# Optimization experiments

Hardware: AMD Instinct MI355X
Metric: run time of the kernel (lower is better)

## Reference

```python
import jax, jax.numpy as jnp
import numpy as np
from jax import lax

B, T, D, H, Z, L = 64, 1024, 128, 512, 64, 2

def lstm_layer(x_tbd, h0, c0, Wih, Whh, bih, bhh):
    # x_tbd: [T,B,Din]; precompute input contribution (big GEMM outside scan)
    gx = jnp.einsum('tbd,gd->tbg', x_tbd, Wih) + (bih + bhh)  # [T,B,4H]
    def step(carry, gxt):
        h, c = carry
        gates = gxt + h @ Whh.T
        i, f, g, o = jnp.split(gates, 4, axis=-1)
        c = jax.nn.sigmoid(f) * c + jax.nn.sigmoid(i) * jnp.tanh(g)
        h = jax.nn.sigmoid(o) * jnp.tanh(c)
        return (h, c), h
    (hT, cT), hs = lax.scan(step, (h0, c0), gx)
    return hs, hT, cT  # hs: [T,B,H]

def run_lstm(x_btd, h0_l, c0_l, params):
    # params: list of (Wih, Whh, bih, bhh) per layer; h0_l/c0_l: [L,B,H]
    seq = jnp.transpose(x_btd, (1, 0, 2))
    hTs = []
    for l, (Wih, Whh, bih, bhh) in enumerate(params):
        seq, hT, cT = lstm_layer(seq, h0_l[l], c0_l[l], Wih, Whh, bih, bhh)
        hTs.append(hT)
    return jnp.transpose(seq, (1, 0, 2)), jnp.stack(hTs)

def setup_inputs() -> dict:
    key = jax.random.key(0)
    ks = iter(jax.random.split(key, 32))
    s = 0.05
    d = {'x': jax.random.uniform(next(ks), (B, T, D), jnp.float32)}
    for pre in ('enc', 'dec'):
        for l in range(L):
            din = D if l == 0 else H
            d[f'{pre}_Wih{l}'] = jax.random.normal(next(ks), (4 * H, din), jnp.float32) * s
            d[f'{pre}_Whh{l}'] = jax.random.normal(next(ks), (4 * H, H), jnp.float32) * s
            d[f'{pre}_bih{l}'] = jnp.zeros((4 * H,), jnp.float32)
            d[f'{pre}_bhh{l}'] = jnp.zeros((4 * H,), jnp.float32)
    d['tl_W'] = jax.random.normal(next(ks), (Z, H), jnp.float32) * s
    d['tl_b'] = jnp.zeros((Z,), jnp.float32)
    d['lh_W'] = jax.random.normal(next(ks), (H * L, Z), jnp.float32) * s
    d['lh_b'] = jnp.zeros((H * L,), jnp.float32)
    d['op_W'] = jax.random.normal(next(ks), (D, H), jnp.float32) * s
    d['op_b'] = jnp.zeros((D,), jnp.float32)
    return d

def reference(x, enc_Wih0, enc_Whh0, enc_bih0, enc_bhh0, enc_Wih1, enc_Whh1, enc_bih1, enc_bhh1,
              dec_Wih0, dec_Whh0, dec_bih0, dec_bhh0, dec_Wih1, dec_Whh1, dec_bih1, dec_bhh1,
              tl_W, tl_b, lh_W, lh_b, op_W, op_b):
    enc_p = [(enc_Wih0, enc_Whh0, enc_bih0, enc_bhh0), (enc_Wih1, enc_Whh1, enc_bih1, enc_bhh1)]
    dec_p = [(dec_Wih0, dec_Whh0, dec_bih0, dec_bhh0), (dec_Wih1, dec_Whh1, dec_bih1, dec_bhh1)]
    zeros_lbh = jnp.zeros((L, B, H), x.dtype)
    # encode
    _, h_n = run_lstm(x, zeros_lbh, zeros_lbh, enc_p)
    z = h_n[-1] @ tl_W.T + tl_b  # [B,Z]
    # decode: zero input sequence, latent-derived initial hidden state
    init_h = jnp.tanh(z @ lh_W.T + lh_b).reshape(B, L, H).transpose(1, 0, 2)  # matches torch .view(L,B,H)? no
    init_h = jnp.tanh(z @ lh_W.T + lh_b).reshape(L, B, H)  # torch: view(num_layers, batch, hidden) on [B, H*L] flat -- faithful to source
    dec_in = jnp.zeros((B, T, D), x.dtype)
    dec_out, _ = run_lstm(dec_in, init_h, jnp.zeros_like(init_h), dec_p)
    recon = jax.nn.sigmoid(jnp.einsum('bth,dh->btd', dec_out, op_W) + op_b)
    return recon, z
```

## Files before the change

kernel.cpp:

```cpp
#include <hip/hip_runtime.h>
#include <cstdint>
#include <cstddef>

typedef unsigned short u16;
typedef unsigned int u32;
typedef __attribute__((ext_vector_type(8))) short short8;
typedef __attribute__((ext_vector_type(4))) float f32x4;

#define AGENT_SCOPE __HIP_MEMORY_SCOPE_AGENT
#define SPIN_CAP 20000000
#define POLL_CAP 200000
#define SENT 0xFFFFFFFFu

__device__ __forceinline__ u16 f2bf(float f) {
  u32 u = __float_as_uint(f);
  return (u16)((u + 0x7FFFu + ((u >> 16) & 1u)) >> 16);
}
__device__ __forceinline__ float bf2f(u16 s) { return __uint_as_float(((u32)s) << 16); }
__device__ __forceinline__ float sigm(float x) { return 1.f / (1.f + __expf(-x)); }
__device__ __forceinline__ float tanha(float x) { return 1.f - 2.f / (__expf(2.f * x) + 1.f); }
__device__ __forceinline__ void wait_vm0() { asm volatile("s_waitcnt vmcnt(0)" ::: "memory"); }
__device__ __forceinline__ u32 um(u32 a, u32 b) { return a > b ? a : b; }

__device__ __forceinline__ uint4 ldx4(const void* p) {
  uint4 r;
  asm volatile("global_load_dwordx4 %0, %1, off sc0 sc1" : "=v"(r) : "v"(p) : "memory");
  return r;
}

__global__ void __launch_bounds__(256, 1)
lstm_ae_kernel(const float* __restrict__ x,
    const float* __restrict__ eWih0, const float* __restrict__ eWhh0,
    const float* __restrict__ ebi0,  const float* __restrict__ ebh0,
    const float* __restrict__ eWih1, const float* __restrict__ eWhh1,
    const float* __restrict__ ebi1,  const float* __restrict__ ebh1,
    const float* __restrict__ dWhh0,
    const float* __restrict__ dbi0,  const float* __restrict__ dbh0,
    const float* __restrict__ dWih1, const float* __restrict__ dWhh1,
    const float* __restrict__ dbi1,  const float* __restrict__ dbh1,
    const float* __restrict__ tlW,   const float* __restrict__ tlb,
    const float* __restrict__ lhW,   const float* __restrict__ lhb,
    const float* __restrict__ opW,   const float* __restrict__ opb,
    float* __restrict__ out, char* __restrict__ wsb)
{
  __shared__ __align__(16) u16 sH0[16 * 520];
  __shared__ __align__(16) u16 sH1[16 * 520];
  __shared__ __align__(16) u16 sX[16 * 136];
  __shared__ __align__(16) u16 sOPW[2 * 520];
  __shared__ float sP[4 * 256];
  __shared__ float sBias[64];
  __shared__ float sC[256];
  __shared__ float sZ[16 * 64];
  __shared__ float sOPB[4];

  u32* gcnt  = (u32*)wsb;
  float* zbuf= (float*)(wsb + 4096);
  u32* h0r   = (u32*)(wsb + 32768);
  u32* h1r   = (u32*)(wsb + 229376);

  const int tid  = threadIdx.x;
  const int col  = blockIdx.x & 3;
  const int rowg = blockIdx.x >> 2;
  const int wid  = tid >> 6;
  const int lane = tid & 63;
  const int m    = lane & 15;
  const int qo   = (lane >> 4) * 8;

  auto stage_slot = [&](int q0, int q1, bool p0on, bool p1on) {
    const char* base0 = (const char*)(h0r + ((q0 * 4 + col) << 12)) + tid * 16;
    const char* base1 = (const char*)(h1r + ((q1 * 4 + col) << 12)) + tid * 16;
    uint4 v0[4], v1[4];
    bool d0 = !p0on, d1 = !p1on;
    int it = 0;
    for (;;) {
      if (!d0) {
        #pragma unroll
        for (int i = 0; i < 4; ++i) v0[i] = ldx4(base0 + i * 4096);
      }
      if (!d1) {
        #pragma unroll
        for (int i = 0; i < 4; ++i) v1[i] = ldx4(base1 + i * 4096);
      }
      asm volatile("s_waitcnt vmcnt(0)" ::: "memory");
      __builtin_amdgcn_sched_barrier(0);
      if (!d0) {
        u32 mx = 0;
        #pragma unroll
        for (int i = 0; i < 4; ++i)
          mx = um(mx, um(um(v0[i].x, v0[i].y), um(v0[i].z, v0[i].w)));
        d0 = (mx != SENT);
      }
      if (!d1) {
        u32 mx = 0;
        #pragma unroll
        for (int i = 0; i < 4; ++i)
          mx = um(mx, um(um(v1[i].x, v1[i].y), um(v1[i].z, v1[i].w)));
        d1 = (mx != SENT);
      }
      if ((d0 && d1) || ++it >= POLL_CAP) break;
      __builtin_amdgcn_s_sleep(4);
    }
    u32* dH0 = (u32*)sH0; u32* dH1 = (u32*)sH1;
    const int db = (tid & 15) * 260 + (tid >> 4) * 4;
    if (p0on) {
      #pragma unroll
      for (int i = 0; i < 4; ++i) *(uint4*)(dH0 + db + i * 64) = v0[i];
    }
    if (p1on) {
      #pragma unroll
      for (int i = 0; i < 4; ++i) *(uint4*)(dH1 + db + i * 64) = v1[i];
    }
  };

  auto clears = [&](int s) {
    if (tid < 64) {
      int cq0 = (s + 1) % 3, cq1 = s % 3;
      __hip_atomic_store(h0r + ((cq0 * 4 + col) << 12) + (rowg << 6) + tid,
                         SENT, __ATOMIC_RELAXED, AGENT_SCOPE);
      __hip_atomic_store(h1r + ((cq1 * 4 + col) << 12) + (rowg << 6) + tid,
                         SENT, __ATOMIC_RELAXED, AGENT_SCOPE);
    }
  };

  auto stage_xt = [&](int s) {
    int b = tid >> 4, seg = tid & 15;
    const float* p = x + (size_t)(col * 16 + b) * 131072 + (size_t)s * 128 + seg * 8;
    float4 f0 = *(const float4*)p, f1 = *(const float4*)(p + 4);
    uint4 v;
    v.x = (u32)f2bf(f0.x) | ((u32)f2bf(f0.y) << 16);
    v.y = (u32)f2bf(f0.z) | ((u32)f2bf(f0.w) << 16);
    v.z = (u32)f2bf(f1.x) | ((u32)f2bf(f1.y) << 16);
    v.w = (u32)f2bf(f1.z) | ((u32)f2bf(f1.w) << 16);
    *(uint4*)(sX + b * 136 + seg * 8) = v;
  };

  auto ldw = [&](const float* W, int ld, int row, int kofs) -> short8 {
    const float* p = W + (size_t)row * ld + kofs + qo;
    float4 f0 = *(const float4*)p, f1 = *(const float4*)(p + 4);
    short8 r;
    r[0] = (short)f2bf(f0.x); r[1] = (short)f2bf(f0.y);
    r[2] = (short)f2bf(f0.z); r[3] = (short)f2bf(f0.w);
    r[4] = (short)f2bf(f1.x); r[5] = (short)f2bf(f1.y);
    r[6] = (short)f2bf(f1.z); r[7] = (short)f2bf(f1.w);
    return r;
  };

  auto act_store = [&](bool L0a, bool L1a, int q0, int q1) {
    int li = tid >> 7, b = (tid >> 3) & 15, u = tid & 7;
    bool actv = li ? L1a : L0a;
    float hv = 0.f;
    if (actv) {
      float gi = sP[(li*2)*256   + b*16 + u]     + sBias[li*32 + u];
      float gf = sP[(li*2)*256   + b*16 + 8 + u] + sBias[li*32 + 8 + u];
      float gg = sP[(li*2+1)*256 + b*16 + u]     + sBias[li*32 + 16 + u];
      float go = sP[(li*2+1)*256 + b*16 + 8 + u] + sBias[li*32 + 24 + u];
      float c = sC[(li*16 + b)*8 + u];
      c = sigm(gf)*c + sigm(gi)*tanha(gg);
      sC[(li*16 + b)*8 + u] = c;
      hv = sigm(go)*tanha(c);
    }
    u16 hb = f2bf(hv);
    u32 other = __shfl_xor((u32)hb, 1);
    if (actv && !(u & 1)) {
      u32 v = (u32)hb | (other << 16);
      u32* ring = li ? h1r : h0r;
      int q = li ? q1 : q0;
      __hip_atomic_store(ring + ((q * 4 + col) << 12) + (rowg << 6) + b * 4 + (u >> 1),
                         v, __ATOMIC_RELAXED, AGENT_SCOPE);
    }
  };

  auto gbar = [&](u32 target) {
    __syncthreads();
    if (tid == 0) {
      __hip_atomic_fetch_add(gcnt, 1u, __ATOMIC_RELEASE, AGENT_SCOPE);
      int it = 0;
      while (__hip_atomic_load(gcnt, __ATOMIC_RELAXED, AGENT_SCOPE) < target && ++it < SPIN_CAP) {}
      (void)__hip_atomic_load(gcnt, __ATOMIC_ACQUIRE, AGENT_SCOPE);
    }
    __syncthreads();
  };

  const int nl = (wid & 1) * 16 + m;
  const int gw = ((nl >> 3) << 9) + rowg * 8 + (nl & 7);

  short8 wb[32];

  if (wid < 2) {
    #pragma unroll
    for (int t = 0; t < 4; ++t)  wb[t]      = ldw(eWih0, 128, gw, t * 32);
    #pragma unroll
    for (int t = 0; t < 16; ++t) wb[4 + t]  = ldw(eWhh0, 512, gw, t * 32);
  } else {
    #pragma unroll
    for (int t = 0; t < 16; ++t) wb[t]      = ldw(eWih1, 512, gw, t * 32);
    #pragma unroll
    for (int t = 0; t < 16; ++t) wb[16 + t] = ldw(eWhh1, 512, gw, t * 32);
  }
  if (tid < 64) {
    int li = tid >> 5, n = tid & 31;
    int g = ((n >> 3) << 9) + rowg * 8 + (n & 7);
    sBias[li * 32 + n] = li ? (ebi1[g] + ebh1[g]) : (ebi0[g] + ebh0[g]);
  }
  sC[tid] = 0.f;
  __syncthreads();

  for (int s = 0; s <= 1024; ++s) {
    const bool L0 = (s < 1024), L1 = (s >= 1);
    if (L0) stage_xt(s);
    stage_slot((s + 2) % 3, (s + 1) % 3, true, s >= 1);
    __syncthreads();
    clears(s);

    f32x4 acc = {0.f, 0.f, 0.f, 0.f};
    if (wid < 2) {
      if (L0) {
        #pragma unroll
        for (int t = 0; t < 4; ++t) {
          short8 a = *(const short8*)(sX + m * 136 + t * 32 + qo);
          acc = __builtin_amdgcn_mfma_f32_16x16x32_bf16(a, wb[t], acc, 0, 0, 0);
        }
        #pragma unroll
        for (int t = 0; t < 16; ++t) {
          short8 a = *(const short8*)(sH0 + m * 520 + t * 32 + qo);
          acc = __builtin_amdgcn_mfma_f32_16x16x32_bf16(a, wb[4 + t], acc, 0, 0, 0);
        }
      }
    } else {
      if (L1) {
        #pragma unroll
        for (int t = 0; t < 16; ++t) {
          short8 a = *(const short8*)(sH0 + m * 520 + t * 32 + qo);
          acc = __builtin_amdgcn_mfma_f32_16x16x32_bf16(a, wb[t], acc, 0, 0, 0);
        }
        #pragma unroll
        for (int t = 0; t < 16; ++t) {
          short8 a = *(const short8*)(sH1 + m * 520 + t * 32 + qo);
          acc = __builtin_amdgcn_mfma_f32_16x16x32_bf16(a, wb[16 + t], acc, 0, 0, 0);
        }
      }
    }
    {
      bool wact = (wid < 2) ? L0 : L1;
      if (wact) {
        int mb = (lane >> 4) * 4;
        #pragma unroll
        for (int r = 0; r < 4; ++r) sP[wid * 256 + (mb + r) * 16 + m] = acc[r];
      }
    }
    __syncthreads();
    {
      wait_vm0();
    }
    act_store(L0, L1, s % 3, (s + 2) % 3);
  }

  {
    const u32* b1 = h1r + ((0 * 4 + col) << 12) + tid;
    u32 v1[16];
    int it = 0; bool ok = false;
    while (!ok && it++ < POLL_CAP) {
      ok = true;
      #pragma unroll
      for (int i = 0; i < 16; ++i) {
        v1[i] = __hip_atomic_load(b1 + i * 256, __ATOMIC_RELAXED, AGENT_SCOPE);
        ok &= (v1[i] != SENT);
      }
    }
    u32* dH1 = (u32*)sH1;
    #pragma unroll
    for (int i = 0; i < 16; ++i) {
      int g = i * 256 + tid;
      dH1[((g >> 2) & 15) * 260 + (g >> 6) * 4 + (g & 3)] = v1[i];
    }
  }
  __syncthreads();
  if (tid < 16) {
    int b = tid;
    float acc = tlb[rowg];
    for (int kk = 0; kk < 512; kk += 8) {
      short8 hv = *(const short8*)(sH1 + b * 520 + kk);
      #pragma unroll
      for (int j = 0; j < 8; ++j) acc += bf2f((u16)hv[j]) * tlW[rowg * 512 + kk + j];
    }
    int gb = col * 16 + b;
    __hip_atomic_store((u32*)zbuf + gb * 64 + rowg, __float_as_uint(acc),
                       __ATOMIC_RELAXED, AGENT_SCOPE);
    out[8388608 + gb * 64 + rowg] = acc;
  }
  gbar(256);

  if (tid < 64) {
    #pragma unroll
    for (int q = 0; q < 3; ++q) {
      __hip_atomic_store(h0r + ((q * 4 + col) << 12) + (rowg << 6) + tid,
                         SENT, __ATOMIC_RELAXED, AGENT_SCOPE);
      __hip_atomic_store(h1r + ((q * 4 + col) << 12) + (rowg << 6) + tid,
                         SENT, __ATOMIC_RELAXED, AGENT_SCOPE);
    }
  }
  wait_vm0();

  if (wid < 2) {
    #pragma unroll
    for (int t = 0; t < 16; ++t) wb[t] = ldw(dWhh0, 512, gw, t * 32);
  } else {
    #pragma unroll
    for (int t = 0; t < 16; ++t) wb[t]      = ldw(dWih1, 512, gw, t * 32);
    #pragma unroll
    for (int t = 0; t < 16; ++t) wb[16 + t] = ldw(dWhh1, 512, gw, t * 32);
  }
  if (tid < 64) {
    int li = tid >> 5, n = tid & 31;
    int g = ((n >> 3) << 9) + rowg * 8 + (n & 7);
    sBias[li * 32 + n] = li ? (dbi1[g] + dbh1[g]) : (dbi0[g] + dbh0[g]);
  }
  for (int i = tid; i < 2 * 64; i += 256) {
    int dd = i >> 6, k = (i & 63) * 8;
    const float* p = opW + (size_t)(rowg * 2 + dd) * 512 + k;
    float4 f0 = *(const float4*)p, f1 = *(const float4*)(p + 4);
    uint4 v;
    v.x = (u32)f2bf(f0.x) | ((u32)f2bf(f0.y) << 16);
    v.y = (u32)f2bf(f0.z) | ((u32)f2bf(f0.w) << 16);
    v.z = (u32)f2bf(f1.x) | ((u32)f2bf(f1.y) << 16);
    v.w = (u32)f2bf(f1.z) | ((u32)f2bf(f1.w) << 16);
    *(uint4*)(sOPW + dd * 520 + k) = v;
  }
  if (tid < 2) sOPB[tid] = opb[rowg * 2 + tid];
  sC[tid] = 0.f;

  {
    int ri = tid >> 4, kk = (tid & 15) * 4;
    int zr = ((ri >> 3) << 5) + 8 * col + (ri & 7);
    #pragma unroll
    for (int j = 0; j < 4; ++j)
      sZ[ri * 64 + kk + j] = __uint_as_float(
          __hip_atomic_load((u32*)zbuf + zr * 64 + kk + j, __ATOMIC_RELAXED, AGENT_SCOPE));
  }
  __syncthreads();
  {
    int li = tid >> 7, hh = (tid >> 4) & 7, qb = (tid >> 3) & 1, u = tid & 7;
    int cc = qb * 512 + rowg * 8 + u;
    int bl = 2 * hh + qb;
    float acc2 = lhb[cc];
    const float* lw = lhW + (size_t)cc * 64;
    #pragma unroll 8
    for (int k = 0; k < 64; ++k) acc2 += sZ[(li * 8 + hh) * 64 + k] * lw[k];
    u16 hb = f2bf(tanha(acc2));
    u32 other = __shfl_xor((u32)hb, 1);
    if (!(u & 1)) {
      u32 v = (u32)hb | (other << 16);
      u32* ring = li ? h1r : h0r;
      __hip_atomic_store(ring + ((2 * 4 + col) << 12) + (rowg << 6) + bl * 4 + (u >> 1),
                         v, __ATOMIC_RELAXED, AGENT_SCOPE);
    }
  }
  gbar(512);

  for (int s = 0; s <= 1025; ++s) {
    const bool L0 = (s < 1024), L1 = (s >= 1 && s <= 1024), RC = (s >= 2);
    stage_slot((s + 2) % 3, (s + 1) % 3, s <= 1024, s >= 1);
    __syncthreads();
    clears(s);

    f32x4 acc = {0.f, 0.f, 0.f, 0.f};
    if (wid < 2) {
      if (L0) {
        #pragma unroll
        for (int t = 0; t < 16; ++t) {
          short8 a = *(const short8*)(sH0 + m * 520 + t * 32 + qo);
          acc = __builtin_amdgcn_mfma_f32_16x16x32_bf16(a, wb[t], acc, 0, 0, 0);
        }
      }
    } else {
      if (L1) {
        #pragma unroll
        for (int t = 0; t < 16; ++t) {
          short8 a = *(const short8*)(sH0 + m * 520 + t * 32 + qo);
          acc = __builtin_amdgcn_mfma_f32_16x16x32_bf16(a, wb[t], acc, 0, 0, 0);
        }
        #pragma unroll
        for (int t = 0; t < 16; ++t) {
          short8 a = *(const short8*)(sH1 + m * 520 + t * 32 + qo);
          acc = __builtin_amdgcn_mfma_f32_16x16x32_bf16(a, wb[16 + t], acc, 0, 0, 0);
        }
      }
    }
    {
      bool wact = (wid < 2) ? L0 : L1;
      if (wact) {
        int mb = (lane >> 4) * 4;
        #pragma unroll
        for (int r = 0; r < 4; ++r) sP[wid * 256 + (mb + r) * 16 + m] = acc[r];
      }
    }
    __syncthreads();
    wait_vm0();
    act_store(L0, L1, s % 3, (s + 2) % 3);

    if (RC) {
      __syncthreads();
      int b = tid >> 4, dd = (tid >> 3) & 1, pt = tid & 7;
      float acc2 = 0.f;
      int k0 = pt * 64;
      for (int kk = 0; kk < 64; kk += 8) {
        short8 hv = *(const short8*)(sH1 + b * 520 + k0 + kk);
        short8 wv = *(const short8*)(sOPW + dd * 520 + k0 + kk);
        #pragma unroll
        for (int j = 0; j < 8; ++j) acc2 += bf2f((u16)hv[j]) * bf2f((u16)wv[j]);
      }
      sP[tid] = acc2;
      __syncthreads();
      if (tid < 32) {
        int b2 = tid >> 1, d2 = tid & 1;
        float sum = sOPB[d2];
        #pragma unroll
        for (int j = 0; j < 8; ++j) sum += sP[b2 * 16 + d2 * 8 + j];
        out[(size_t)(col * 16 + b2) * 131072 + (size_t)(s - 2) * 128 + rowg * 2 + d2]
            = sigm(sum);
      }
    }
  }
}

extern "C" void kernel_launch(void* const* d_in, const int* in_sizes, int n_in,
                              void* d_out, int out_size, void* d_ws, size_t ws_size,
                              hipStream_t stream) {
  (void)in_sizes; (void)n_in; (void)out_size; (void)ws_size;
  char* ws = (char*)d_ws;
  hipMemsetAsync(ws, 0, 32768, stream);
  hipMemsetAsync(ws + 32768, 0xFF, 131072, stream);
  hipMemsetAsync(ws + 163840, 0x00, 65536, stream);
  hipMemsetAsync(ws + 229376, 0xFF, 131072, stream);
  hipMemsetAsync(ws + 360448, 0x00, 65536, stream);
  lstm_ae_kernel<<<dim3(256), dim3(256), 0, stream>>>(
      (const float*)d_in[0],
      (const float*)d_in[1],  (const float*)d_in[2],
      (const float*)d_in[3],  (const float*)d_in[4],
      (const float*)d_in[5],  (const float*)d_in[6],
      (const float*)d_in[7],  (const float*)d_in[8],
      (const float*)d_in[10],
      (const float*)d_in[11], (const float*)d_in[12],
      (const float*)d_in[13], (const float*)d_in[14],
      (const float*)d_in[15], (const float*)d_in[16],
      (const float*)d_in[17], (const float*)d_in[18],
      (const float*)d_in[19], (const float*)d_in[20],
      (const float*)d_in[21], (const float*)d_in[22],
      (float*)d_out, (char*)d_ws);
}
```

Measured before the change: 5.209 ms.

## Keep gate outputs in registers and double-buffer hidden state to cut per-step barriers

Swaps the MFMA operand order and reorders weight rows so each lane holds i,f,g,o for one (batch, unit) pair. The LSTM cell update can then run in registers without an sP scratch round-trip and its extra __syncthreads. The hidden-state LDS buffers are double-buffered by step parity, so the next step's staging does not need a barrier after compute. The output projection moves to MFMA on an otherwise idle wave, and two MFMA accumulator chains replace one serial chain. It also halves the poll cap and adds sleep to the global barrier spin, which risks slower wakeup and premature cap exits.

Result: slower. 5.787 ms (+11.1%).

```diff
diff --git a/kernel.cpp b/kernel.cpp
--- a/kernel.cpp
+++ b/kernel.cpp
@@ -9,7 +9,7 @@
 
 #define AGENT_SCOPE __HIP_MEMORY_SCOPE_AGENT
 #define SPIN_CAP 20000000
-#define POLL_CAP 200000
+#define POLL_CAP 100000
 #define SENT 0xFFFFFFFFu
 
 __device__ __forceinline__ u16 f2bf(float f) {
@@ -43,15 +43,9 @@
     const float* __restrict__ opW,   const float* __restrict__ opb,
     float* __restrict__ out, char* __restrict__ wsb)
 {
-  __shared__ __align__(16) u16 sH0[16 * 520];
-  __shared__ __align__(16) u16 sH1[16 * 520];
+  __shared__ __align__(16) u16 sH[2][2][16 * 520];
   __shared__ __align__(16) u16 sX[16 * 136];
-  __shared__ __align__(16) u16 sOPW[2 * 520];
-  __shared__ float sP[4 * 256];
-  __shared__ float sBias[64];
-  __shared__ float sC[256];
   __shared__ float sZ[16 * 64];
-  __shared__ float sOPB[4];
 
   u32* gcnt  = (u32*)wsb;
   float* zbuf= (float*)(wsb + 4096);
@@ -64,9 +58,24 @@
   const int wid  = tid >> 6;
   const int lane = tid & 63;
   const int m    = lane & 15;
-  const int qo   = (lane >> 4) * 8;
-
-  auto stage_slot = [&](int q0, int q1, bool p0on, bool p1on) {
+  const int q    = lane >> 4;
+  const int qo   = q * 8;
+  const int li   = wid >> 1;
+  const int hf   = wid & 1;
+
+  const int wrA = (m & 3) * 512 + rowg * 8 + hf * 4 + (m >> 2);
+
+  auto cvt8 = [&](const float* p) -> short8 {
+    float4 f0 = *(const float4*)p, f1 = *(const float4*)(p + 4);
+    short8 r;
+    r[0] = (short)f2bf(f0.x); r[1] = (short)f2bf(f0.y);
+    r[2] = (short)f2bf(f0.z); r[3] = (short)f2bf(f0.w);
+    r[4] = (short)f2bf(f1.x); r[5] = (short)f2bf(f1.y);
+    r[6] = (short)f2bf(f1.z); r[7] = (short)f2bf(f1.w);
+    return r;
+  };
+
+  auto stage_slot = [&](int q0, int q1, bool p0on, bool p1on, int p) {
     const char* base0 = (const char*)(h0r + ((q0 * 4 + col) << 12)) + tid * 16;
     const char* base1 = (const char*)(h1r + ((q1 * 4 + col) << 12)) + tid * 16;
     uint4 v0[4], v1[4];
@@ -100,7 +109,7 @@
       if ((d0 && d1) || ++it >= POLL_CAP) break;
       __builtin_amdgcn_s_sleep(4);
     }
-    u32* dH0 = (u32*)sH0; u32* dH1 = (u32*)sH1;
+    u32* dH0 = (u32*)sH[p][0]; u32* dH1 = (u32*)sH[p][1];
     const int db = (tid & 15) * 260 + (tid >> 4) * 4;
     if (p0on) {
       #pragma unroll
@@ -134,143 +143,125 @@
     *(uint4*)(sX + b * 136 + seg * 8) = v;
   };
 
-  auto ldw = [&](const float* W, int ld, int row, int kofs) -> short8 {
-    const float* p = W + (size_t)row * ld + kofs + qo;
-    float4 f0 = *(const float4*)p, f1 = *(const float4*)(p + 4);
-    short8 r;
-    r[0] = (short)f2bf(f0.x); r[1] = (short)f2bf(f0.y);
-    r[2] = (short)f2bf(f0.z); r[3] = (short)f2bf(f0.w);
-    r[4] = (short)f2bf(f1.x); r[5] = (short)f2bf(f1.y);
-    r[6] = (short)f2bf(f1.z); r[7] = (short)f2bf(f1.w);
-    return r;
-  };
-
-  auto act_store = [&](bool L0a, bool L1a, int q0, int q1) {
-    int li = tid >> 7, b = (tid >> 3) & 15, u = tid & 7;
-    bool actv = li ? L1a : L0a;
-    float hv = 0.f;
-    if (actv) {
-      float gi = sP[(li*2)*256   + b*16 + u]     + sBias[li*32 + u];
-      float gf = sP[(li*2)*256   + b*16 + 8 + u] + sBias[li*32 + 8 + u];
-      float gg = sP[(li*2+1)*256 + b*16 + u]     + sBias[li*32 + 16 + u];
-      float go = sP[(li*2+1)*256 + b*16 + 8 + u] + sBias[li*32 + 24 + u];
-      float c = sC[(li*16 + b)*8 + u];
-      c = sigm(gf)*c + sigm(gi)*tanha(gg);
-      sC[(li*16 + b)*8 + u] = c;
-      hv = sigm(go)*tanha(c);
-    }
-    u16 hb = f2bf(hv);
-    u32 other = __shfl_xor((u32)hb, 1);
-    if (actv && !(u & 1)) {
-      u32 v = (u32)hb | (other << 16);
-      u32* ring = li ? h1r : h0r;
-      int q = li ? q1 : q0;
-      __hip_atomic_store(ring + ((q * 4 + col) << 12) + (rowg << 6) + b * 4 + (u >> 1),
-                         v, __ATOMIC_RELAXED, AGENT_SCOPE);
-    }
-  };
-
   auto gbar = [&](u32 target) {
     __syncthreads();
     if (tid == 0) {
       __hip_atomic_fetch_add(gcnt, 1u, __ATOMIC_RELEASE, AGENT_SCOPE);
       int it = 0;
-      while (__hip_atomic_load(gcnt, __ATOMIC_RELAXED, AGENT_SCOPE) < target && ++it < SPIN_CAP) {}
+      while (__hip_atomic_load(gcnt, __ATOMIC_RELAXED, AGENT_SCOPE) < target && ++it < SPIN_CAP) {
+        __builtin_amdgcn_s_sleep(8);
+      }
       (void)__hip_atomic_load(gcnt, __ATOMIC_ACQUIRE, AGENT_SCOPE);
     }
     __syncthreads();
   };
 
-  const int nl = (wid & 1) * 16 + m;
-  const int gw = ((nl >> 3) << 9) + rowg * 8 + (nl & 7);
-
-  short8 wb[32];
-
-  if (wid < 2) {
-    #pragma unroll
-    for (int t = 0; t < 4; ++t)  wb[t]      = ldw(eWih0, 128, gw, t * 32);
-    #pragma unroll
-    for (int t = 0; t < 16; ++t) wb[4 + t]  = ldw(eWhh0, 512, gw, t * 32);
+  float cst = 0.f;
+  f32x4 bias = {0.f, 0.f, 0.f, 0.f};
+
+  auto act_store = [&](f32x4 a0, f32x4 a1, int qs) {
+    float gi = a0[0] + a1[0], gf = a0[1] + a1[1];
+    float gg = a0[2] + a1[2], go = a0[3] + a1[3];
+    cst = sigm(gf) * cst + sigm(gi) * tanha(gg);
+    float h = sigm(go) * tanha(cst);
+    u16 hbv = f2bf(h);
+    u32 ph = __shfl_xor((u32)hbv, 16);
+    wait_vm0();
+    if (!(q & 1)) {
+      u32* ring = li ? h1r : h0r;
+      __hip_atomic_store(ring + ((qs * 4 + col) << 12) + (rowg << 6)
+                             + m * 4 + hf * 2 + (q >> 1),
+                         (u32)hbv | (ph << 16), __ATOMIC_RELAXED, AGENT_SCOPE);
+    }
+  };
+
+  short8 wb[32], xw[4];
+
+  if (li == 0) {
+    #pragma unroll
+    for (int t = 0; t < 4; ++t)  xw[t] = cvt8(eWih0 + (size_t)wrA * 128 + t * 32 + qo);
+    #pragma unroll
+    for (int t = 0; t < 16; ++t) wb[t] = cvt8(eWhh0 + (size_t)wrA * 512 + t * 32 + qo);
+    #pragma unroll
+    for (int r = 0; r < 4; ++r) {
+      int wr = r * 512 + rowg * 8 + hf * 4 + q;
+      bias[r] = ebi0[wr] + ebh0[wr];
+    }
   } else {
     #pragma unroll
-    for (int t = 0; t < 16; ++t) wb[t]      = ldw(eWih1, 512, gw, t * 32);
-    #pragma unroll
-    for (int t = 0; t < 16; ++t) wb[16 + t] = ldw(eWhh1, 512, gw, t * 32);
-  }
-  if (tid < 64) {
-    int li = tid >> 5, n = tid & 31;
-    int g = ((n >> 3) << 9) + rowg * 8 + (n & 7);
-    sBias[li * 32 + n] = li ? (ebi1[g] + ebh1[g]) : (ebi0[g] + ebh0[g]);
-  }
-  sC[tid] = 0.f;
+    for (int t = 0; t < 16; ++t) wb[t]      = cvt8(eWih1 + (size_t)wrA * 512 + t * 32 + qo);
+    #pragma unroll
+    for (int t = 0; t < 16; ++t) wb[16 + t] = cvt8(eWhh1 + (size_t)wrA * 512 + t * 32 + qo);
+    #pragma unroll
+    for (int r = 0; r < 4; ++r) {
+      int wr = r * 512 + rowg * 8 + hf * 4 + q;
+      bias[r] = ebi1[wr] + ebh1[wr];
+    }
+  }
   __syncthreads();
 
   for (int s = 0; s <= 1024; ++s) {
     const bool L0 = (s < 1024), L1 = (s >= 1);
+    const int p = s & 1;
     if (L0) stage_xt(s);
-    stage_slot((s + 2) % 3, (s + 1) % 3, true, s >= 1);
+    stage_slot((s + 2) % 3, (s + 1) % 3, true, s >= 1, p);
     __syncthreads();
     clears(s);
 
-    f32x4 acc = {0.f, 0.f, 0.f, 0.f};
-    if (wid < 2) {
-      if (L0) {
+    const u16* hb0 = sH[p][0];
+    const u16* hb1 = sH[p][1];
+    const bool active = li ? L1 : L0;
+    if (active) {
+      f32x4 a0 = bias, a1 = {0.f, 0.f, 0.f, 0.f};
+      if (li == 0) {
         #pragma unroll
         for (int t = 0; t < 4; ++t) {
-          short8 a = *(const short8*)(sX + m * 136 + t * 32 + qo);
-          acc = __builtin_amdgcn_mfma_f32_16x16x32_bf16(a, wb[t], acc, 0, 0, 0);
-        }
-        #pragma unroll
-        for (int t = 0; t < 16; ++t) {
-          short8 a = *(const short8*)(sH0 + m * 520 + t * 32 + qo);
-          acc = __builtin_amdgcn_mfma_f32_16x16x32_bf16(a, wb[4 + t], acc, 0, 0, 0);
-        }
-      }
-    } else {
-      if (L1) {
-        #pragma unroll
-        for (int t = 0; t < 16; ++t) {
-          short8 a = *(const short8*)(sH0 + m * 520 + t * 32 + qo);
-          acc = __builtin_amdgcn_mfma_f32_16x16x32_bf16(a, wb[t], acc, 0, 0, 0);
-        }
-        #pragma unroll
-        for (int t = 0; t < 16; ++t) {
-          short8 a = *(const short8*)(sH1 + m * 520 + t * 32 + qo);
-          acc = __builtin_amdgcn_mfma_f32_16x16x32_bf16(a, wb[16 + t], acc, 0, 0, 0);
-        }
-      }
-    }
-    {
-      bool wact = (wid < 2) ? L0 : L1;
-      if (wact) {
-        int mb = (lane >> 4) * 4;
-        #pragma unroll
-        for (int r = 0; r < 4; ++r) sP[wid * 256 + (mb + r) * 16 + m] = acc[r];
-      }
-    }
-    __syncthreads();
-    {
-      wait_vm0();
-    }
-    act_store(L0, L1, s % 3, (s + 2) % 3);
-  }
-
-  {
+          short8 xa = *(const short8*)(sX + m * 136 + t * 32 + qo);
+          if (t & 1) a1 = __builtin_amdgcn_mfma_f32_16x16x32_bf16(xw[t], xa, a1, 0, 0, 0);
+          else       a0 = __builtin_amdgcn_mfma_f32_16x16x32_bf16(xw[t], xa, a0, 0, 0, 0);
+        }
+        #pragma unroll
+        for (int t = 0; t < 16; ++t) {
+          short8 ha = *(const short8*)(hb0 + m * 520 + t * 32 + qo);
+          if (t & 1) a1 = __builtin_amdgcn_mfma_f32_16x16x32_bf16(wb[t], ha, a1, 0, 0, 0);
+          else       a0 = __builtin_amdgcn_mfma_f32_16x16x32_bf16(wb[t], ha, a0, 0, 0, 0);
+        }
+        act_store(a0, a1, s % 3);
+      } else {
+        #pragma unroll
+        for (int t = 0; t < 16; ++t) {
+          short8 ha = *(const short8*)(hb0 + m * 520 + t * 32 + qo);
+          if (t & 1) a1 = __builtin_amdgcn_mfma_f32_16x16x32_bf16(wb[t], ha, a1, 0, 0, 0);
+          else       a0 = __builtin_amdgcn_mfma_f32_16x16x32_bf16(wb[t], ha, a0, 0, 0, 0);
+        }
+        #pragma unroll
+        for (int t = 0; t < 16; ++t) {
+          short8 ha = *(const short8*)(hb1 + m * 520 + t * 32 + qo);
+          if (t & 1) a1 = __builtin_amdgcn_mfma_f32_16x16x32_bf16(wb[16 + t], ha, a1, 0, 0, 0);
+          else       a0 = __builtin_amdgcn_mfma_f32_16x16x32_bf16(wb[16 + t], ha, a0, 0, 0, 0);
+        }
+        act_store(a0, a1, (s + 2) % 3);
+      }
+    }
+  }
+
+  u16* sH1z = sH[1][1];
+  if (tid < 128) {
     const u32* b1 = h1r + ((0 * 4 + col) << 12) + tid;
-    u32 v1[16];
+    u32 v1[32];
     int it = 0; bool ok = false;
     while (!ok && it++ < POLL_CAP) {
       ok = true;
       #pragma unroll
-      for (int i = 0; i < 16; ++i) {
-        v1[i] = __hip_atomic_load(b1 + i * 256, __ATOMIC_RELAXED, AGENT_SCOPE);
+      for (int i = 0; i < 32; ++i) {
+        v1[i] = __hip_atomic_load(b1 + i * 128, __ATOMIC_RELAXED, AGENT_SCOPE);
         ok &= (v1[i] != SENT);
       }
     }
-    u32* dH1 = (u32*)sH1;
-    #pragma unroll
-    for (int i = 0; i < 16; ++i) {
-      int g = i * 256 + tid;
+    u32* dH1 = (u32*)sH1z;
+    #pragma unroll
+    for (int i = 0; i < 32; ++i) {
+      int g = i * 128 + tid;
       dH1[((g >> 2) & 15) * 260 + (g >> 6) * 4 + (g & 3)] = v1[i];
     }
   }
@@ -279,7 +270,7 @@
     int b = tid;
     float acc = tlb[rowg];
     for (int kk = 0; kk < 512; kk += 8) {
-      short8 hv = *(const short8*)(sH1 + b * 520 + kk);
+      short8 hv = *(const short8*)(sH1z + b * 520 + kk);
       #pragma unroll
       for (int j = 0; j < 8; ++j) acc += bf2f((u16)hv[j]) * tlW[rowg * 512 + kk + j];
     }
@@ -292,42 +283,44 @@
 
   if (tid < 64) {
     #pragma unroll
-    for (int q = 0; q < 3; ++q) {
-      __hip_atomic_store(h0r + ((q * 4 + col) << 12) + (rowg << 6) + tid,
+    for (int qq = 0; qq < 3; ++qq) {
+      __hip_atomic_store(h0r + ((qq * 4 + col) << 12) + (rowg << 6) + tid,
                          SENT, __ATOMIC_RELAXED, AGENT_SCOPE);
-      __hip_atomic_store(h1r + ((q * 4 + col) << 12) + (rowg << 6) + tid,
+      __hip_atomic_store(h1r + ((qq * 4 + col) << 12) + (rowg << 6) + tid,
                          SENT, __ATOMIC_RELAXED, AGENT_SCOPE);
     }
   }
   wait_vm0();
 
-  if (wid < 2) {
-    #pragma unroll
-    for (int t = 0; t < 16; ++t) wb[t] = ldw(dWhh0, 512, gw, t * 32);
+  short8 rcw[16];
+  float opbA = 0.f, opbB = 0.f;
+  if (li == 0) {
+    #pragma unroll
+    for (int t = 0; t < 16; ++t) wb[t] = cvt8(dWhh0 + (size_t)wrA * 512 + t * 32 + qo);
+    #pragma unroll
+    for (int r = 0; r < 4; ++r) {
+      int wr = r * 512 + rowg * 8 + hf * 4 + q;
+      bias[r] = dbi0[wr] + dbh0[wr];
+    }
+    if (hf == 1) {
+      const short8 z8 = {0, 0, 0, 0, 0, 0, 0, 0};
+      #pragma unroll
+      for (int t = 0; t < 16; ++t)
+        rcw[t] = (m < 2) ? cvt8(opW + (size_t)(rowg * 2 + m) * 512 + t * 32 + qo) : z8;
+      opbA = opb[rowg * 2]; opbB = opb[rowg * 2 + 1];
+    }
   } else {
     #pragma unroll
-    for (int t = 0; t < 16; ++t) wb[t]      = ldw(dWih1, 512, gw, t * 32);
-    #pragma unroll
-    for (int t = 0; t < 16; ++t) wb[16 + t] = ldw(dWhh1, 512, gw, t * 32);
-  }
-  if (tid < 64) {
-    int li = tid >> 5, n = tid & 31;
-    int g = ((n >> 3) << 9) + rowg * 8 + (n & 7);
-    sBias[li * 32 + n] = li ? (dbi1[g] + dbh1[g]) : (dbi0[g] + dbh0[g]);
-  }
-  for (int i = tid; i < 2 * 64; i += 256) {
-    int dd = i >> 6, k = (i & 63) * 8;
-    const float* p = opW + (size_t)(rowg * 2 + dd) * 512 + k;
-    float4 f0 = *(const float4*)p, f1 = *(const float4*)(p + 4);
-    uint4 v;
-    v.x = (u32)f2bf(f0.x) | ((u32)f2bf(f0.y) << 16);
-    v.y = (u32)f2bf(f0.z) | ((u32)f2bf(f0.w) << 16);
-    v.z = (u32)f2bf(f1.x) | ((u32)f2bf(f1.y) << 16);
-    v.w = (u32)f2bf(f1.z) | ((u32)f2bf(f1.w) << 16);
-    *(uint4*)(sOPW + dd * 520 + k) = v;
-  }
-  if (tid < 2) sOPB[tid] = opb[rowg * 2 + tid];
-  sC[tid] = 0.f;
+    for (int t = 0; t < 16; ++t) wb[t]      = cvt8(dWih1 + (size_t)wrA * 512 + t * 32 + qo);
+    #pragma unroll
+    for (int t = 0; t < 16; ++t) wb[16 + t] = cvt8(dWhh1 + (size_t)wrA * 512 + t * 32 + qo);
+    #pragma unroll
+    for (int r = 0; r < 4; ++r) {
+      int wr = r * 512 + rowg * 8 + hf * 4 + q;
+      bias[r] = dbi1[wr] + dbh1[wr];
+    }
+  }
+  cst = 0.f;
 
   {
     int ri = tid >> 4, kk = (tid & 15) * 4;
@@ -339,18 +332,18 @@
   }
   __syncthreads();
   {
-    int li = tid >> 7, hh = (tid >> 4) & 7, qb = (tid >> 3) & 1, u = tid & 7;
+    int lli = tid >> 7, hh = (tid >> 4) & 7, qb = (tid >> 3) & 1, u = tid & 7;
     int cc = qb * 512 + rowg * 8 + u;
     int bl = 2 * hh + qb;
     float acc2 = lhb[cc];
     const float* lw = lhW + (size_t)cc * 64;
     #pragma unroll 8
-    for (int k = 0; k < 64; ++k) acc2 += sZ[(li * 8 + hh) * 64 + k] * lw[k];
-    u16 hb = f2bf(tanha(acc2));
-    u32 other = __shfl_xor((u32)hb, 1);
+    for (int k = 0; k < 64; ++k) acc2 += sZ[(lli * 8 + hh) * 64 + k] * lw[k];
+    u16 hbv = f2bf(tanha(acc2));
+    u32 other = __shfl_xor((u32)hbv, 1);
     if (!(u & 1)) {
-      u32 v = (u32)hb | (other << 16);
-      u32* ring = li ? h1r : h0r;
+      u32 v = (u32)hbv | (other << 16);
+      u32* ring = lli ? h1r : h0r;
       __hip_atomic_store(ring + ((2 * 4 + col) << 12) + (rowg << 6) + bl * 4 + (u >> 1),
                          v, __ATOMIC_RELAXED, AGENT_SCOPE);
     }
@@ -359,65 +352,54 @@
 
   for (int s = 0; s <= 1025; ++s) {
     const bool L0 = (s < 1024), L1 = (s >= 1 && s <= 1024), RC = (s >= 2);
-    stage_slot((s + 2) % 3, (s + 1) % 3, s <= 1024, s >= 1);
+    const int p = s & 1;
+    stage_slot((s + 2) % 3, (s + 1) % 3, s <= 1024, s >= 1, p);
     __syncthreads();
     clears(s);
 
-    f32x4 acc = {0.f, 0.f, 0.f, 0.f};
-    if (wid < 2) {
+    const u16* hb0 = sH[p][0];
+    const u16* hb1 = sH[p][1];
+    if (li == 0) {
       if (L0) {
-        #pragma unroll
-        for (int t = 0; t < 16; ++t) {
-          short8 a = *(const short8*)(sH0 + m * 520 + t * 32 + qo);
-          acc = __builtin_amdgcn_mfma_f32_16x16x32_bf16(a, wb[t], acc, 0, 0, 0);
+        f32x4 a0 = bias, a1 = {0.f, 0.f, 0.f, 0.f};
+        #pragma unroll
+        for (int t = 0; t < 16; ++t) {
+          short8 ha = *(const short8*)(hb0 + m * 520 + t * 32 + qo);
+          if (t & 1) a1 = __builtin_amdgcn_mfma_f32_16x16x32_bf16(wb[t], ha, a1, 0, 0, 0);
+          else       a0 = __builtin_amdgcn_mfma_f32_16x16x32_bf16(wb[t], ha, a0, 0, 0, 0);
+        }
+        act_store(a0, a1, s % 3);
+      }
+      if (hf == 1 && RC) {
+        f32x4 r0 = {0.f, 0.f, 0.f, 0.f}, r1 = {0.f, 0.f, 0.f, 0.f};
+        #pragma unroll
+        for (int t = 0; t < 16; ++t) {
+          short8 ha = *(const short8*)(hb1 + m * 520 + t * 32 + qo);
+          if (t & 1) r1 = __builtin_amdgcn_mfma_f32_16x16x32_bf16(rcw[t], ha, r1, 0, 0, 0);
+          else       r0 = __builtin_amdgcn_mfma_f32_16x16x32_bf16(rcw[t], ha, r0, 0, 0, 0);
+        }
+        if (q == 0) {
+          size_t ob = (size_t)(col * 16 + m) * 131072 + (size_t)(s - 2) * 128 + rowg * 2;
+          out[ob]     = sigm(r0[0] + r1[0] + opbA);
+          out[ob + 1] = sigm(r0[1] + r1[1] + opbB);
         }
       }
     } else {
       if (L1) {
-        #pragma unroll
-        for (int t = 0; t < 16; ++t) {
-          short8 a = *(const short8*)(sH0 + m * 520 + t * 32 + qo);
-          acc = __builtin_amdgcn_mfma_f32_16x16x32_bf16(a, wb[t], acc, 0, 0, 0);
-        }
-        #pragma unroll
-        for (int t = 0; t < 16; ++t) {
-          short8 a = *(const short8*)(sH1 + m * 520 + t * 32 + qo);
-          acc = __builtin_amdgcn_mfma_f32_16x16x32_bf16(a, wb[16 + t], acc, 0, 0, 0);
-        }
-      }
-    }
-    {
-      bool wact = (wid < 2) ? L0 : L1;
-      if (wact) {
-        int mb = (lane >> 4) * 4;
-        #pragma unroll
-        for (int r = 0; r < 4; ++r) sP[wid * 256 + (mb + r) * 16 + m] = acc[r];
-      }
-    }
-    __syncthreads();
-    wait_vm0();
-    act_store(L0, L1, s % 3, (s + 2) % 3);
-
-    if (RC) {
-      __syncthreads();
-      int b = tid >> 4, dd = (tid >> 3) & 1, pt = tid & 7;
-      float acc2 = 0.f;
-      int k0 = pt * 64;
-      for (int kk = 0; kk < 64; kk += 8) {
-        short8 hv = *(const short8*)(sH1 + b * 520 + k0 + kk);
-        short8 wv = *(const short8*)(sOPW + dd * 520 + k0 + kk);
-        #pragma unroll
-        for (int j = 0; j < 8; ++j) acc2 += bf2f((u16)hv[j]) * bf2f((u16)wv[j]);
-      }
-      sP[tid] = acc2;
-      __syncthreads();
-      if (tid < 32) {
-        int b2 = tid >> 1, d2 = tid & 1;
-        float sum = sOPB[d2];
-        #pragma unroll
-        for (int j = 0; j < 8; ++j) sum += sP[b2 * 16 + d2 * 8 + j];
-        out[(size_t)(col * 16 + b2) * 131072 + (size_t)(s - 2) * 128 + rowg * 2 + d2]
-            = sigm(sum);
+        f32x4 a0 = bias, a1 = {0.f, 0.f, 0.f, 0.f};
+        #pragma unroll
+        for (int t = 0; t < 16; ++t) {
+          short8 ha = *(const short8*)(hb0 + m * 520 + t * 32 + qo);
+          if (t & 1) a1 = __builtin_amdgcn_mfma_f32_16x16x32_bf16(wb[t], ha, a1, 0, 0, 0);
+          else       a0 = __builtin_amdgcn_mfma_f32_16x16x32_bf16(wb[t], ha, a0, 0, 0, 0);
+        }
+        #pragma unroll
+        for (int t = 0; t < 16; ++t) {
+          short8 ha = *(const short8*)(hb1 + m * 520 + t * 32 + qo);
+          if (t & 1) a1 = __builtin_amdgcn_mfma_f32_16x16x32_bf16(wb[16 + t], ha, a1, 0, 0, 0);
+          else       a0 = __builtin_amdgcn_mfma_f32_16x16x32_bf16(wb[16 + t], ha, a0, 0, 0, 0);
+        }
+        act_store(a0, a1, (s + 2) % 3);
       }
     }
   }
```

## Pipeline ring polling with double-buffered loads and vectorize ring stores

Applied to the files above, without the earlier changes.

Replaces the per-step flag polling of the hidden-state rings with a two-buffer rotating load scheme for the layer-0 ring and a separate sleep-poll loop for the layer-1 ring. The `__all` wave vote is used to decide readiness, and the fixed s_sleep between polls is removed. Hidden-state publishes and sentinel clears now go out as single 16-byte stores per 8 units instead of many 4-byte atomic stores, with shuffles to gather the values. The goal is lower cross-block handoff latency on the recurrent critical path, at the cost of more outstanding memory traffic and more subtle ordering with the vmcnt waits.

Measured after the change: 5.385 ms. +3.4%, slower.

```diff
diff --git a/kernel.cpp b/kernel.cpp
--- a/kernel.cpp
+++ b/kernel.cpp
@@ -6,10 +6,11 @@
 typedef unsigned int u32;
 typedef __attribute__((ext_vector_type(8))) short short8;
 typedef __attribute__((ext_vector_type(4))) float f32x4;
+typedef __attribute__((ext_vector_type(4))) unsigned int u32x4;
 
 #define AGENT_SCOPE __HIP_MEMORY_SCOPE_AGENT
 #define SPIN_CAP 20000000
-#define POLL_CAP 200000
+#define POLL_CAP 100000
 #define SENT 0xFFFFFFFFu
 
 __device__ __forceinline__ u16 f2bf(float f) {
@@ -22,10 +23,13 @@
 __device__ __forceinline__ void wait_vm0() { asm volatile("s_waitcnt vmcnt(0)" ::: "memory"); }
 __device__ __forceinline__ u32 um(u32 a, u32 b) { return a > b ? a : b; }
 
-__device__ __forceinline__ uint4 ldx4(const void* p) {
-  uint4 r;
+__device__ __forceinline__ u32x4 ldx4(const void* p) {
+  u32x4 r;
   asm volatile("global_load_dwordx4 %0, %1, off sc0 sc1" : "=v"(r) : "v"(p) : "memory");
   return r;
+}
+__device__ __forceinline__ void stx4(void* p, u32x4 v) {
+  asm volatile("global_store_dwordx4 %0, %1, off sc0 sc1" :: "v"(p), "v"(v) : "memory");
 }
 
 __global__ void __launch_bounds__(256, 1)
@@ -69,56 +73,104 @@
   auto stage_slot = [&](int q0, int q1, bool p0on, bool p1on) {
     const char* base0 = (const char*)(h0r + ((q0 * 4 + col) << 12)) + tid * 16;
     const char* base1 = (const char*)(h1r + ((q1 * 4 + col) << 12)) + tid * 16;
-    uint4 v0[4], v1[4];
-    bool d0 = !p0on, d1 = !p1on;
+    u32x4 A[4], Bv[4], v1[4];
+    wait_vm0();
+    __builtin_amdgcn_sched_barrier(0);
+    bool okH1 = !p1on, h1ck = !p1on;
     int it = 0;
-    for (;;) {
-      if (!d0) {
-        #pragma unroll
-        for (int i = 0; i < 4; ++i) v0[i] = ldx4(base0 + i * 4096);
-      }
-      if (!d1) {
+    if (p0on) {
+      #pragma unroll
+      for (int i = 0; i < 4; ++i) A[i] = ldx4(base0 + i * 4096);
+      if (p1on) {
         #pragma unroll
         for (int i = 0; i < 4; ++i) v1[i] = ldx4(base1 + i * 4096);
       }
-      asm volatile("s_waitcnt vmcnt(0)" ::: "memory");
+      #pragma unroll
+      for (int i = 0; i < 4; ++i) Bv[i] = ldx4(base0 + i * 4096);
+      bool tookB = false;
+      for (;;) {
+        asm volatile("s_waitcnt vmcnt(4)" ::: "memory");
+        __builtin_amdgcn_sched_barrier(0);
+        if (!h1ck) {
+          u32 mx = 0;
+          #pragma unroll
+          for (int i = 0; i < 4; ++i)
+            mx = um(mx, um(um(v1[i].x, v1[i].y), um(v1[i].z, v1[i].w)));
+          okH1 = __all(mx != SENT);
+          h1ck = true;
+        }
+        u32 ma = 0;
+        #pragma unroll
+        for (int i = 0; i < 4; ++i)
+          ma = um(ma, um(um(A[i].x, A[i].y), um(A[i].z, A[i].w)));
+        if (__all(ma != SENT)) break;
+        if (++it >= POLL_CAP) break;
+        #pragma unroll
+        for (int i = 0; i < 4; ++i) A[i] = ldx4(base0 + i * 4096);
+        asm volatile("s_waitcnt vmcnt(4)" ::: "memory");
+        __builtin_amdgcn_sched_barrier(0);
+        u32 mb = 0;
+        #pragma unroll
+        for (int i = 0; i < 4; ++i)
+          mb = um(mb, um(um(Bv[i].x, Bv[i].y), um(Bv[i].z, Bv[i].w)));
+        if (__all(mb != SENT)) { tookB = true; break; }
+        if (++it >= POLL_CAP) break;
+        #pragma unroll
+        for (int i = 0; i < 4; ++i) Bv[i] = ldx4(base0 + i * 4096);
+      }
+      wait_vm0();
       __builtin_amdgcn_sched_barrier(0);
-      if (!d0) {
-        u32 mx = 0;
-        #pragma unroll
-        for (int i = 0; i < 4; ++i)
-          mx = um(mx, um(um(v0[i].x, v0[i].y), um(v0[i].z, v0[i].w)));
-        d0 = (mx != SENT);
-      }
-      if (!d1) {
-        u32 mx = 0;
-        #pragma unroll
-        for (int i = 0; i < 4; ++i)
-          mx = um(mx, um(um(v1[i].x, v1[i].y), um(v1[i].z, v1[i].w)));
-        d1 = (mx != SENT);
-      }
-      if ((d0 && d1) || ++it >= POLL_CAP) break;
-      __builtin_amdgcn_s_sleep(4);
+      if (tookB) {
+        #pragma unroll
+        for (int i = 0; i < 4; ++i) A[i] = Bv[i];
+      }
+    } else if (p1on) {
+      #pragma unroll
+      for (int i = 0; i < 4; ++i) v1[i] = ldx4(base1 + i * 4096);
+    }
+    if (!h1ck) {
+      wait_vm0();
+      __builtin_amdgcn_sched_barrier(0);
+      u32 mx = 0;
+      #pragma unroll
+      for (int i = 0; i < 4; ++i)
+        mx = um(mx, um(um(v1[i].x, v1[i].y), um(v1[i].z, v1[i].w)));
+      okH1 = __all(mx != SENT);
+      h1ck = true;
+    }
+    while (!okH1) {
+      if (++it >= POLL_CAP) break;
+      __builtin_amdgcn_s_sleep(1);
+      #pragma unroll
+      for (int i = 0; i < 4; ++i) v1[i] = ldx4(base1 + i * 4096);
+      wait_vm0();
+      __builtin_amdgcn_sched_barrier(0);
+      u32 mx = 0;
+      #pragma unroll
+      for (int i = 0; i < 4; ++i)
+        mx = um(mx, um(um(v1[i].x, v1[i].y), um(v1[i].z, v1[i].w)));
+      okH1 = __all(mx != SENT);
     }
     u32* dH0 = (u32*)sH0; u32* dH1 = (u32*)sH1;
     const int db = (tid & 15) * 260 + (tid >> 4) * 4;
     if (p0on) {
       #pragma unroll
-      for (int i = 0; i < 4; ++i) *(uint4*)(dH0 + db + i * 64) = v0[i];
+      for (int i = 0; i < 4; ++i) *(u32x4*)(dH0 + db + i * 64) = A[i];
     }
     if (p1on) {
       #pragma unroll
-      for (int i = 0; i < 4; ++i) *(uint4*)(dH1 + db + i * 64) = v1[i];
+      for (int i = 0; i < 4; ++i) *(u32x4*)(dH1 + db + i * 64) = v1[i];
     }
   };
 
   auto clears = [&](int s) {
-    if (tid < 64) {
+    if (tid < 32) {
       int cq0 = (s + 1) % 3, cq1 = s % 3;
-      __hip_atomic_store(h0r + ((cq0 * 4 + col) << 12) + (rowg << 6) + tid,
-                         SENT, __ATOMIC_RELAXED, AGENT_SCOPE);
-      __hip_atomic_store(h1r + ((cq1 * 4 + col) << 12) + (rowg << 6) + tid,
-                         SENT, __ATOMIC_RELAXED, AGENT_SCOPE);
+      u32x4 sv = {SENT, SENT, SENT, SENT};
+      if (tid < 16)
+        stx4(h0r + ((cq0 * 4 + col) << 12) + (rowg << 6) + tid * 4, sv);
+      else
+        stx4(h1r + ((cq1 * 4 + col) << 12) + (rowg << 6) + (tid - 16) * 4, sv);
     }
   };
 
@@ -145,7 +197,7 @@
     return r;
   };
 
-  auto act_store = [&](bool L0a, bool L1a, int q0, int q1) {
+  auto act_store = [&](bool L0a, bool L1a, int q0s, int q1s) {
     int li = tid >> 7, b = (tid >> 3) & 15, u = tid & 7;
     bool actv = li ? L1a : L0a;
     float hv = 0.f;
@@ -160,13 +212,16 @@
       hv = sigm(go)*tanha(c);
     }
     u16 hb = f2bf(hv);
-    u32 other = __shfl_xor((u32)hb, 1);
-    if (actv && !(u & 1)) {
-      u32 v = (u32)hb | (other << 16);
+    u32 dw  = (u32)hb | (__shfl_xor((u32)hb, 1) << 16);
+    u32 dwB = __shfl_xor(dw, 2);
+    u32 dwC = __shfl_xor(dw, 4);
+    u32 dwD = __shfl_xor(dwB, 4);
+    wait_vm0();
+    if (actv && u == 0) {
       u32* ring = li ? h1r : h0r;
-      int q = li ? q1 : q0;
-      __hip_atomic_store(ring + ((q * 4 + col) << 12) + (rowg << 6) + b * 4 + (u >> 1),
-                         v, __ATOMIC_RELAXED, AGENT_SCOPE);
+      int qq = li ? q1s : q0s;
+      u32x4 v = {dw, dwB, dwC, dwD};
+      stx4(ring + ((qq * 4 + col) << 12) + (rowg << 6) + b * 4, v);
     }
   };
 
@@ -249,9 +304,6 @@
       }
     }
     __syncthreads();
-    {
-      wait_vm0();
-    }
     act_store(L0, L1, s % 3, (s + 2) % 3);
   }
 
@@ -395,7 +447,6 @@
       }
     }
     __syncthreads();
-    wait_vm0();
     act_store(L0, L1, s % 3, (s + 2) % 3);
 
     if (RC) {
@@ -428,11 +479,11 @@
                               hipStream_t stream) {
   (void)in_sizes; (void)n_in; (void)out_size; (void)ws_size;
   char* ws = (char*)d_ws;
-  hipMemsetAsync(ws, 0, 32768, stream);
-  hipMemsetAsync(ws + 32768, 0xFF, 131072, stream);
-  hipMemsetAsync(ws + 163840, 0x00, 65536, stream);
-  hipMemsetAsync(ws + 229376, 0xFF, 131072, stream);
-  hipMemsetAsync(ws + 360448, 0x00, 65536, stream);
+  (void)hipMemsetAsync(ws, 0, 32768, stream);
+  (void)hipMemsetAsync(ws + 32768, 0xFF, 131072, stream);
+  (void)hipMemsetAsync(ws + 163840, 0x00, 65536, stream);
+  (void)hipMemsetAsync(ws + 229376, 0xFF, 131072, stream);
+  (void)hipMemsetAsync(ws + 360448, 0x00, 65536, stream);
   lstm_ae_kernel<<<dim3(256), dim3(256), 0, stream>>>(
       (const float*)d_in[0],
       (const float*)d_in[1],  (const float*)d_in[2],
```
